# Optimization experiments

Measured on AMD Instinct MI355X. Metric: run time of the kernel, lower is better.

Reference implementation:

```python
import jax, jax.numpy as jnp
import numpy as np

CAPACITY_FACTOR = 1.25


def setup_inputs() -> dict:
    key = jax.random.key(0)
    k1, k2, k3, k4, k5, k6 = jax.random.split(key, 6)
    N, d, E, h = 8192, 1024, 8, 2816
    x = jax.random.normal(k1, (N, d), dtype=jnp.float32)
    topK_indices = jax.random.randint(k2, (N,), 0, E, dtype=jnp.int64)
    topK_scores = jax.random.uniform(k3, (N,), dtype=jnp.float32)
    Wg = jax.random.normal(k4, (E, d, h), dtype=jnp.float32) * 0.02
    Wu = jax.random.normal(k5, (E, d, h), dtype=jnp.float32) * 0.02
    Wd = jax.random.normal(k6, (E, h, d), dtype=jnp.float32) * 0.02
    return {"x": x, "topK_indices": topK_indices, "topK_scores": topK_scores,
            "Wg": Wg, "Wu": Wu, "Wd": Wd}


def reference(x, topK_indices, topK_scores, Wg, Wu, Wd):
    # x: [N, d] tokens; topK_indices: [N] top-1 expert ids; per-expert SwiGLU FFN.
    N, d = x.shape
    E = Wg.shape[0]
    capacity = int(CAPACITY_FACTOR * N / E)  # = 1280

    idx = topK_indices.astype(jnp.int32)
    onehot = jax.nn.one_hot(idx, E, dtype=jnp.int32)            # [N, E]
    # position of each token within its expert's queue (first-come-first-served)
    pos = jnp.sum((jnp.cumsum(onehot, axis=0) - 1) * onehot, axis=1)  # [N]
    kept = pos < capacity                                        # dropped tokens pass through

    # flat dispatch slot: expert*capacity + pos for kept tokens, overflow bucket otherwise
    slots = jnp.where(kept, idx * capacity + pos, E * capacity)  # [N]
    buf = jnp.zeros((E * capacity + 1, d), dtype=x.dtype).at[slots].set(x)
    xe = buf[: E * capacity].reshape(E, capacity, d)             # [E, C, d]

    # per-expert SwiGLU FFN (grouped GEMMs)
    hgate = jnp.einsum('ecd,edh->ech', xe, Wg)
    hup = jnp.einsum('ecd,edh->ech', xe, Wu)
    hact = jax.nn.silu(hgate) * hup
    out = jnp.einsum('ech,ehd->ecd', hact, Wd).reshape(E * capacity, d)
    out = jnp.concatenate([out, jnp.zeros((1, d), out.dtype)], axis=0)

    y_tok = out[slots]                                           # gather back per token
    # multiply_gate_scores=True: scale expert output by routing score; dropped -> identity
    y = jnp.where(kept[:, None], y_tok * topK_scores[:, None], x)
    return y
```

## Files before the change

kernel.cpp:

```cpp
#include <hip/hip_runtime.h>
#include <cstdint>
#include <cstddef>

#define N_TOK 8192
#define DIM   1024
#define NEXP  8
#define HID   2816
#define CAP   1280

typedef __bf16 bf16x8 __attribute__((ext_vector_type(8)));
typedef float  floatx4 __attribute__((ext_vector_type(4)));
typedef unsigned short u16x8 __attribute__((ext_vector_type(8)));

__device__ __forceinline__ unsigned short f2bf(float f) {
  return __builtin_bit_cast(unsigned short, (__bf16)f);
}

__device__ __forceinline__ void async16(void* lds, const void* g) {
  __builtin_amdgcn_global_load_lds(
      (const __attribute__((address_space(1))) void*)g,
      (__attribute__((address_space(3))) void*)lds, 16, 0, 0);
}

__device__ __forceinline__ void fence_barrier() {
  asm volatile("" ::: "memory");
  __builtin_amdgcn_s_barrier();
  asm volatile("" ::: "memory");
}

__device__ __forceinline__ floatx4 mfma16(bf16x8 a, bf16x8 b, floatx4 c) {
  return __builtin_amdgcn_mfma_f32_16x16x32_bf16(a, b, c, 0, 0, 0);
}

__global__ void route_kernel(const int* __restrict__ idx, int idx_stride,
                             int* __restrict__ slot,
                             int* __restrict__ slot_token,
                             int* __restrict__ counts) {
  __shared__ int hist[256][NEXP];
  const int t = threadIdx.x;
  int loc[NEXP];
#pragma unroll
  for (int e = 0; e < NEXP; e++) loc[e] = 0;
  const int base = t * 32;
  for (int i = 0; i < 32; i++) {
    const int e = idx[(base + i) * idx_stride];
#pragma unroll
    for (int k = 0; k < NEXP; k++) loc[k] += (e == k) ? 1 : 0;
  }
  int v[NEXP];
#pragma unroll
  for (int e = 0; e < NEXP; e++) { v[e] = loc[e]; hist[t][e] = loc[e]; }
  __syncthreads();
  for (int d = 1; d < 256; d <<= 1) {
    int nb[NEXP];
    const bool has = (t >= d);
    if (has) {
#pragma unroll
      for (int e = 0; e < NEXP; e++) nb[e] = hist[t - d][e];
    }
    __syncthreads();
    if (has) {
#pragma unroll
      for (int e = 0; e < NEXP; e++) { v[e] += nb[e]; hist[t][e] = v[e]; }
    }
    __syncthreads();
  }
  if (t < NEXP) {
    const int tot = hist[255][t];
    counts[t] = tot < CAP ? tot : CAP;
  }
  int b2[NEXP];
#pragma unroll
  for (int e = 0; e < NEXP; e++) b2[e] = v[e] - loc[e];
  for (int i = 0; i < 32; i++) {
    const int n = base + i;
    const int e = idx[n * idx_stride];
    int p = 0;
#pragma unroll
    for (int k = 0; k < NEXP; k++) {
      if (e == k) { p = b2[k]; b2[k] = p + 1; }
    }
    if (p < CAP) {
      const int s = e * CAP + p;
      slot[n] = s;
      slot_token[s] = n;
    } else {
      slot[n] = -1;
    }
  }
}

__global__ void dispatch_kernel(const float* __restrict__ x,
                                const int* __restrict__ slot,
                                unsigned short* __restrict__ xe,
                                float* __restrict__ y) {
  const int n = blockIdx.x;
  const int t = threadIdx.x;
  const int s = slot[n];
  const float4 v = ((const float4*)(x + (size_t)n * DIM))[t];
  if (s >= 0) {
    ushort4 b;
    b.x = f2bf(v.x); b.y = f2bf(v.y); b.z = f2bf(v.z); b.w = f2bf(v.w);
    ((ushort4*)(xe + (size_t)s * DIM))[t] = b;
  } else {
    ((float4*)(y + (size_t)n * DIM))[t] = v;
  }
}

__global__ __launch_bounds__(256)
void transpose_cvt(const float* __restrict__ in,
                   unsigned short* __restrict__ out,
                   const int R, const int C) {
  __shared__ float tile[64][65];
  const int e = blockIdx.z;
  const float* ib = in + (size_t)e * R * C;
  unsigned short* ob = out + (size_t)e * R * C;
  const int t = threadIdx.x;
  const int c0 = blockIdx.x * 64, r0 = blockIdx.y * 64;
  const int lr = t >> 4;
  const int lc = (t & 15) * 4;
#pragma unroll
  for (int i = 0; i < 4; i++) {
    const float4 v = *(const float4*)(ib + (size_t)(r0 + lr + i * 16) * C + c0 + lc);
    tile[lr + i * 16][lc + 0] = v.x;
    tile[lr + i * 16][lc + 1] = v.y;
    tile[lr + i * 16][lc + 2] = v.z;
    tile[lr + i * 16][lc + 3] = v.w;
  }
  __syncthreads();
  const int oc = t >> 2;
  const int sub = t & 3;
#pragma unroll
  for (int half = 0; half < 2; half++) {
    const int rch = sub + half * 4;
    u16x8 o;
#pragma unroll
    for (int j = 0; j < 8; j++) o[j] = f2bf(tile[rch * 8 + j][oc]);
    *(u16x8*)(ob + (size_t)(c0 + oc) * R + r0 + rch * 8) = o;
  }
}


__global__ __launch_bounds__(512, 2)
void gateup_gemm4(const unsigned short* __restrict__ A,
                  const unsigned short* __restrict__ Bg,
                  const unsigned short* __restrict__ Bu,
                  const int* __restrict__ counts,
                  unsigned short* __restrict__ hact) {
  extern __shared__ __align__(16) char smem[];
  const int bid = blockIdx.x;
  const int xcd = bid & 7;
  const int slotb = bid >> 3;
  const int m = slotb % 5;
  const int cgl = slotb / 5;
  const int cg = xcd + 8 * cgl;
  const int n = cg % 44;
  const int e = cg / 44;

  const int cnt = counts[e];
  const int m0 = m * 256;
  if (m0 >= cnt) return;
  const int n0 = n * 64;

  const int t = threadIdx.x;
  const int lane = t & 63;
  const int w = t >> 6;
  const int wr = w >> 1;
  const int wc = w & 1;
  const int li = lane & 15;
  const int q = lane >> 4;

  const int cphys = (((li & 1) * 4 + q) ^ (li >> 1)) * 16;
  const int aoff0 = (wr * 32 + (li >> 1)) * 128 + cphys;
  const int boff0 = 16384 + (wc * 16 + (li >> 1)) * 128 + cphys;

  const int clog = (t & 7) ^ ((t >> 3) & 7);
  const int kc = (clog & 3) * 8;
  const int rloc = 2 * (t >> 3) + (clog >> 2);
  const unsigned short* aSrc  = A + ((size_t)e * CAP + m0 + rloc) * DIM + kc;
  const unsigned short* aSrc2 = aSrc + (size_t)128 * DIM;
  const int rB = n0 + 2 * ((t >> 3) & 31) + (clog >> 2);
  const unsigned short* bSrc =
      ((t < 256) ? Bg : Bu) + ((size_t)e * HID + rB) * DIM + kc;

  floatx4 accg[4][2] = {};
  floatx4 accu[4][2] = {};
  bf16x8 fA[8], fB[8];

  constexpr int NTK = DIM / 32;

#define GU_STAGE(TN)                                                        \
  {                                                                         \
    char* bb_ = smem + ((TN) & 3) * 24576;                                  \
    const int ko_ = (TN) * 32;                                              \
    async16(bb_ + t * 16, aSrc + ko_);                                      \
    async16(bb_ + 8192 + t * 16, aSrc2 + ko_);                              \
    async16(bb_ + 16384 + t * 16, bSrc + ko_);                              \
  }

#define GU_READF(DST, TN)                                                   \
  {                                                                         \
    const char* sb_ = smem + ((TN) & 3) * 24576;                            \
    DST[0] = *(const bf16x8*)(sb_ + aoff0);                                 \
    DST[1] = *(const bf16x8*)(sb_ + aoff0 + 1024);                          \
    DST[2] = *(const bf16x8*)(sb_ + aoff0 + 2048);                          \
    DST[3] = *(const bf16x8*)(sb_ + aoff0 + 3072);                          \
    DST[4] = *(const bf16x8*)(sb_ + boff0);                                 \
    DST[5] = *(const bf16x8*)(sb_ + boff0 + 1024);                          \
    DST[6] = *(const bf16x8*)(sb_ + boff0 + 4096);                          \
    DST[7] = *(const bf16x8*)(sb_ + boff0 + 5120);                          \
  }

#define GU_MFMA(CUR)                                                        \
  {                                                                         \
    __builtin_amdgcn_s_setprio(1);                                          \
    _Pragma("unroll")                                                       \
    for (int mi = 0; mi < 4; mi++) {                                        \
      accg[mi][0] = mfma16(CUR[mi], CUR[4], accg[mi][0]);                   \
      accg[mi][1] = mfma16(CUR[mi], CUR[5], accg[mi][1]);                   \
      accu[mi][0] = mfma16(CUR[mi], CUR[6], accu[mi][0]);                   \
      accu[mi][1] = mfma16(CUR[mi], CUR[7], accu[mi][1]);                   \
    }                                                                       \
    __builtin_amdgcn_s_setprio(0);                                          \
  }

#define GU_BODY(TN, CUR, NXT)                                               \
  {                                                                         \
    if ((TN) + 3 < NTK) GU_STAGE((TN) + 3);                                 \
    if ((TN) + 1 < NTK) {                                                   \
      if ((TN) + 3 < NTK)      asm volatile("s_waitcnt vmcnt(6)" ::: "memory"); \
      else if ((TN) + 2 < NTK) asm volatile("s_waitcnt vmcnt(3)" ::: "memory"); \
      else                     asm volatile("s_waitcnt vmcnt(0)" ::: "memory"); \
      fence_barrier();                                                      \
      GU_READF(NXT, (TN) + 1);                                              \
      __builtin_amdgcn_sched_barrier(0);                                    \
    }                                                                       \
    GU_MFMA(CUR);                                                           \
    asm volatile("s_waitcnt lgkmcnt(0)" ::: "memory");                      \
    __builtin_amdgcn_sched_barrier(0);                                      \
  }

  GU_STAGE(0); GU_STAGE(1); GU_STAGE(2);
  asm volatile("s_waitcnt vmcnt(6)" ::: "memory");
  fence_barrier();
  GU_READF(fA, 0);
  asm volatile("s_waitcnt lgkmcnt(0)" ::: "memory");
  __builtin_amdgcn_sched_barrier(0);

  for (int T = 0; T < NTK; T += 2) {
    GU_BODY(T, fA, fB);
    GU_BODY(T + 1, fB, fA);
  }
#undef GU_BODY
#undef GU_MFMA
#undef GU_READF
#undef GU_STAGE

  unsigned short* ob = hact + (size_t)e * CAP * HID;
#pragma unroll
  for (int mi = 0; mi < 4; mi++)
#pragma unroll
    for (int r = 0; r < 4; r++) {
      const int row = m0 + wr * 64 + mi * 16 + q * 4 + r;
      const size_t rb = (size_t)row * HID;
#pragma unroll
      for (int ni = 0; ni < 2; ni++) {
        const int col = n0 + wc * 32 + ni * 16 + li;
        const float g = accg[mi][ni][r];
        const float u = accu[mi][ni][r];
        ob[rb + col] = f2bf(g / (1.0f + __expf(-g)) * u);
      }
    }
}

__global__ __launch_bounds__(256, 2)
void down_gemm4(const unsigned short* __restrict__ Ah,
                const unsigned short* __restrict__ Bt,
                const int* __restrict__ counts,
                const int* __restrict__ slot_token,
                const float* __restrict__ scores,
                float* __restrict__ y) {
  extern __shared__ __align__(16) char smem[];
  const int bid = blockIdx.x;
  const int xcd = bid & 7;
  const int slotb = bid >> 3;
  const int m = slotb % 10;
  const int cgl = slotb / 10;
  const int cg = xcd + 8 * cgl;
  const int n = cg % 8;
  const int e = cg / 8;

  const int cnt = counts[e];
  const int m0 = m * 128;
  if (m0 >= cnt) return;
  const int n0 = n * 128;

  const int t = threadIdx.x;
  const int lane = t & 63;
  const int w = t >> 6;
  const int wr = w >> 1;
  const int wc = w & 1;
  const int li = lane & 15;
  const int q = lane >> 4;

  const int cphys = (((li & 1) * 4 + q) ^ (li >> 1)) * 16;
  const int aoff0 = (wr * 32 + (li >> 1)) * 128 + cphys;
  const int boff0 = 8192 + (wc * 32 + (li >> 1)) * 128 + cphys;

  const int clog = (t & 7) ^ ((t >> 3) & 7);
  const int kc = (clog & 3) * 8;
  const int rloc = 2 * (t >> 3) + (clog >> 2);
  const unsigned short* aSrc  = Ah + ((size_t)e * CAP + m0 + rloc) * HID + kc;
  const unsigned short* aSrc2 = aSrc + (size_t)64 * HID;
  const unsigned short* bSrc  = Bt + ((size_t)e * DIM + n0 + rloc) * HID + kc;
  const unsigned short* bSrc2 = bSrc + (size_t)64 * HID;

  floatx4 acc[4][4] = {};
  bf16x8 fA[8], fB[8];

  constexpr int NTK = HID / 32;

#define DN_STAGE(TN)                                                        \
  {                                                                         \
    char* bb_ = smem + ((TN) & 3) * 16384;                                  \
    const int ko_ = (TN) * 32;                                              \
    async16(bb_ + t * 16, aSrc + ko_);                                      \
    async16(bb_ + 4096 + t * 16, aSrc2 + ko_);                              \
    async16(bb_ + 8192 + t * 16, bSrc + ko_);                               \
    async16(bb_ + 12288 + t * 16, bSrc2 + ko_);                             \
  }

#define DN_READF(DST, TN)                                                   \
  {                                                                         \
    const char* sb_ = smem + ((TN) & 3) * 16384;                            \
    DST[0] = *(const bf16x8*)(sb_ + aoff0);                                 \
    DST[1] = *(const bf16x8*)(sb_ + aoff0 + 1024);                          \
    DST[2] = *(const bf16x8*)(sb_ + aoff0 + 2048);                          \
    DST[3] = *(const bf16x8*)(sb_ + aoff0 + 3072);                          \
    DST[4] = *(const bf16x8*)(sb_ + boff0);                                 \
    DST[5] = *(const bf16x8*)(sb_ + boff0 + 1024);                          \
    DST[6] = *(const bf16x8*)(sb_ + boff0 + 2048);                          \
    DST[7] = *(const bf16x8*)(sb_ + boff0 + 3072);                          \
  }

#define DN_MFMA(CUR)                                                        \
  {                                                                         \
    __builtin_amdgcn_s_setprio(1);                                          \
    _Pragma("unroll")                                                       \
    for (int mi = 0; mi < 4; mi++) {                                        \
      _Pragma("unroll")                                                     \
      for (int ni = 0; ni < 4; ni++)                                        \
        acc[mi][ni] = mfma16(CUR[mi], CUR[4 + ni], acc[mi][ni]);            \
    }                                                                       \
    __builtin_amdgcn_s_setprio(0);                                          \
  }

#define DN_BODY(TN, CUR, NXT)                                               \
  {                                                                         \
    if ((TN) + 3 < NTK) DN_STAGE((TN) + 3);                                 \
    if ((TN) + 1 < NTK) {                                                   \
      if ((TN) + 3 < NTK)      asm volatile("s_waitcnt vmcnt(8)" ::: "memory"); \
      else if ((TN) + 2 < NTK) asm volatile("s_waitcnt vmcnt(4)" ::: "memory"); \
      else                     asm volatile("s_waitcnt vmcnt(0)" ::: "memory"); \
      fence_barrier();                                                      \
      DN_READF(NXT, (TN) + 1);                                              \
      __builtin_amdgcn_sched_barrier(0);                                    \
    }                                                                       \
    DN_MFMA(CUR);                                                           \
    asm volatile("s_waitcnt lgkmcnt(0)" ::: "memory");                      \
    __builtin_amdgcn_sched_barrier(0);                                      \
  }

  DN_STAGE(0); DN_STAGE(1); DN_STAGE(2);
  asm volatile("s_waitcnt vmcnt(8)" ::: "memory");
  fence_barrier();
  DN_READF(fA, 0);
  asm volatile("s_waitcnt lgkmcnt(0)" ::: "memory");
  __builtin_amdgcn_sched_barrier(0);

  for (int T = 0; T < NTK; T += 2) {
    DN_BODY(T, fA, fB);
    DN_BODY(T + 1, fB, fA);
  }
#undef DN_BODY
#undef DN_MFMA
#undef DN_READF
#undef DN_STAGE

#pragma unroll
  for (int mi = 0; mi < 4; mi++)
#pragma unroll
    for (int r = 0; r < 4; r++) {
      const int row = m0 + wr * 64 + mi * 16 + q * 4 + r;
      if (row < cnt) {
        const int tok = slot_token[e * CAP + row];
        const float s = scores[tok];
        float* yr = y + (size_t)tok * DIM;
#pragma unroll
        for (int ni = 0; ni < 4; ni++) {
          const int col = n0 + wc * 64 + ni * 16 + li;
          yr[col] = acc[mi][ni][r] * s;
        }
      }
    }
}

extern "C" void kernel_launch(void* const* d_in, const int* in_sizes, int n_in,
                              void* d_out, int out_size, void* d_ws, size_t ws_size,
                              hipStream_t stream) {
  const float* x      = (const float*)d_in[0];
  const int*   idx    = (const int*)d_in[1];
  const float* scores = (const float*)d_in[2];
  const float* Wg     = (const float*)d_in[3];
  const float* Wu     = (const float*)d_in[4];
  const float* Wd     = (const float*)d_in[5];
  float* y = (float*)d_out;

  const int idx_stride = (in_sizes[1] == 2 * N_TOK) ? 2 : 1;

  char* ws = (char*)d_ws;
  size_t off = 0;
  auto alloc = [&](size_t b) -> char* {
    char* p = ws + off;
    off += (b + 255) & ~(size_t)255;
    return p;
  };
  int* counts            = (int*)alloc(NEXP * 4);
  int* slot              = (int*)alloc((size_t)N_TOK * 4);
  int* slot_token        = (int*)alloc((size_t)NEXP * CAP * 4);
  unsigned short* xe     = (unsigned short*)alloc((size_t)NEXP * CAP * DIM * 2);
  unsigned short* hact   = (unsigned short*)alloc((size_t)NEXP * CAP * HID * 2);
  unsigned short* wg_t   = (unsigned short*)alloc((size_t)NEXP * DIM * HID * 2);
  unsigned short* wu_t   = (unsigned short*)alloc((size_t)NEXP * DIM * HID * 2);
  unsigned short* wd_t   = (unsigned short*)alloc((size_t)NEXP * DIM * HID * 2);
  (void)ws_size; (void)n_in; (void)out_size;

  static bool s_attr_done = false;
  if (!s_attr_done) {
    hipFuncSetAttribute((const void*)gateup_gemm4,
                        hipFuncAttributeMaxDynamicSharedMemorySize, 98304);
    hipFuncSetAttribute((const void*)down_gemm4,
                        hipFuncAttributeMaxDynamicSharedMemorySize, 65536);
    s_attr_done = true;
  }

  route_kernel<<<1, 256, 0, stream>>>(idx, idx_stride, slot, slot_token, counts);
  dispatch_kernel<<<N_TOK, 256, 0, stream>>>(x, slot, xe, y);

  transpose_cvt<<<dim3(HID / 64, DIM / 64, NEXP), 256, 0, stream>>>(Wg, wg_t, DIM, HID);
  transpose_cvt<<<dim3(HID / 64, DIM / 64, NEXP), 256, 0, stream>>>(Wu, wu_t, DIM, HID);
  transpose_cvt<<<dim3(DIM / 64, HID / 64, NEXP), 256, 0, stream>>>(Wd, wd_t, HID, DIM);

  gateup_gemm4<<<8 * 44 * 5, 512, 98304, stream>>>(xe, wg_t, wu_t, counts, hact);
  down_gemm4<<<8 * 8 * 10, 256, 65536, stream>>>(hact, wd_t, counts, slot_token, scores, y);
}
```

Before: 561.7 us.

## Widen gate/up tile to 128 cols, triple-buffer both GEMMs, expert-per-XCD mapping

The gate/up GEMM tile grows from 64 to 128 hidden columns with a 2x4 warp layout, so each A tile is reused across twice as many columns and the grid is halved. Both GEMMs move from a 4-stage, double-register-fragment pipeline to a 3-stage LDS ring that loads fragments and issues MFMAs in the same iteration. The down GEMM drops to 48KB of LDS so three blocks can fit per CU. Blocks are remapped so each XCD handles a single expert, which is meant to improve L2 reuse of that expert's weights. In exchange, the gate/up kernel needs more accumulator registers and loses the overlap between fragment reads and MFMAs that the old prefetch scheme gave.

```diff
diff --git a/kernel.cpp b/kernel.cpp
--- a/kernel.cpp
+++ b/kernel.cpp
@@ -142,126 +142,97 @@
 
 
 __global__ __launch_bounds__(512, 2)
-void gateup_gemm4(const unsigned short* __restrict__ A,
+void gateup_gemm5(const unsigned short* __restrict__ A,
                   const unsigned short* __restrict__ Bg,
                   const unsigned short* __restrict__ Bu,
                   const int* __restrict__ counts,
                   unsigned short* __restrict__ hact) {
   extern __shared__ __align__(16) char smem[];
   const int bid = blockIdx.x;
-  const int xcd = bid & 7;
-  const int slotb = bid >> 3;
-  const int m = slotb % 5;
-  const int cgl = slotb / 5;
-  const int cg = xcd + 8 * cgl;
-  const int n = cg % 44;
-  const int e = cg / 44;
+  const int e = bid & 7;
+  const int local = bid >> 3;
+  const int n = local / 5;
+  const int m = local % 5;
 
   const int cnt = counts[e];
   const int m0 = m * 256;
   if (m0 >= cnt) return;
-  const int n0 = n * 64;
+  const int n0 = n * 128;
 
   const int t = threadIdx.x;
   const int lane = t & 63;
   const int w = t >> 6;
-  const int wr = w >> 1;
-  const int wc = w & 1;
+  const int wr = w >> 2;
+  const int wc = w & 3;
   const int li = lane & 15;
   const int q = lane >> 4;
 
   const int cphys = (((li & 1) * 4 + q) ^ (li >> 1)) * 16;
-  const int aoff0 = (wr * 32 + (li >> 1)) * 128 + cphys;
-  const int boff0 = 16384 + (wc * 16 + (li >> 1)) * 128 + cphys;
+  const int aoff0 = wr * 8192 + (li >> 1) * 128 + cphys;
+  const int bgoff = 16384 + wc * 2048 + (li >> 1) * 128 + cphys;
+  const int buoff = bgoff + 8192;
 
   const int clog = (t & 7) ^ ((t >> 3) & 7);
   const int kc = (clog & 3) * 8;
   const int rloc = 2 * (t >> 3) + (clog >> 2);
-  const unsigned short* aSrc  = A + ((size_t)e * CAP + m0 + rloc) * DIM + kc;
-  const unsigned short* aSrc2 = aSrc + (size_t)128 * DIM;
-  const int rB = n0 + 2 * ((t >> 3) & 31) + (clog >> 2);
-  const unsigned short* bSrc =
-      ((t < 256) ? Bg : Bu) + ((size_t)e * HID + rB) * DIM + kc;
-
-  floatx4 accg[4][2] = {};
-  floatx4 accu[4][2] = {};
-  bf16x8 fA[8], fB[8];
+  const unsigned short* aS0 = A  + ((size_t)e * CAP + m0 + rloc) * DIM + kc;
+  const unsigned short* aS1 = aS0 + (size_t)128 * DIM;
+  const unsigned short* bgS = Bg + ((size_t)e * HID + n0 + rloc) * DIM + kc;
+  const unsigned short* buS = Bu + ((size_t)e * HID + n0 + rloc) * DIM + kc;
+
+  floatx4 accg[8][2] = {};
+  floatx4 accu[8][2] = {};
 
   constexpr int NTK = DIM / 32;
 
 #define GU_STAGE(TN)                                                        \
   {                                                                         \
-    char* bb_ = smem + ((TN) & 3) * 24576;                                  \
+    char* bb_ = smem + ((TN) % 3) * 32768;                                  \
     const int ko_ = (TN) * 32;                                              \
-    async16(bb_ + t * 16, aSrc + ko_);                                      \
-    async16(bb_ + 8192 + t * 16, aSrc2 + ko_);                              \
-    async16(bb_ + 16384 + t * 16, bSrc + ko_);                              \
-  }
-
-#define GU_READF(DST, TN)                                                   \
-  {                                                                         \
-    const char* sb_ = smem + ((TN) & 3) * 24576;                            \
-    DST[0] = *(const bf16x8*)(sb_ + aoff0);                                 \
-    DST[1] = *(const bf16x8*)(sb_ + aoff0 + 1024);                          \
-    DST[2] = *(const bf16x8*)(sb_ + aoff0 + 2048);                          \
-    DST[3] = *(const bf16x8*)(sb_ + aoff0 + 3072);                          \
-    DST[4] = *(const bf16x8*)(sb_ + boff0);                                 \
-    DST[5] = *(const bf16x8*)(sb_ + boff0 + 1024);                          \
-    DST[6] = *(const bf16x8*)(sb_ + boff0 + 4096);                          \
-    DST[7] = *(const bf16x8*)(sb_ + boff0 + 5120);                          \
-  }
-
-#define GU_MFMA(CUR)                                                        \
-  {                                                                         \
-    __builtin_amdgcn_s_setprio(1);                                          \
-    _Pragma("unroll")                                                       \
-    for (int mi = 0; mi < 4; mi++) {                                        \
-      accg[mi][0] = mfma16(CUR[mi], CUR[4], accg[mi][0]);                   \
-      accg[mi][1] = mfma16(CUR[mi], CUR[5], accg[mi][1]);                   \
-      accu[mi][0] = mfma16(CUR[mi], CUR[6], accu[mi][0]);                   \
-      accu[mi][1] = mfma16(CUR[mi], CUR[7], accu[mi][1]);                   \
-    }                                                                       \
-    __builtin_amdgcn_s_setprio(0);                                          \
-  }
-
-#define GU_BODY(TN, CUR, NXT)                                               \
-  {                                                                         \
-    if ((TN) + 3 < NTK) GU_STAGE((TN) + 3);                                 \
-    if ((TN) + 1 < NTK) {                                                   \
-      if ((TN) + 3 < NTK)      asm volatile("s_waitcnt vmcnt(6)" ::: "memory"); \
-      else if ((TN) + 2 < NTK) asm volatile("s_waitcnt vmcnt(3)" ::: "memory"); \
-      else                     asm volatile("s_waitcnt vmcnt(0)" ::: "memory"); \
-      fence_barrier();                                                      \
-      GU_READF(NXT, (TN) + 1);                                              \
-      __builtin_amdgcn_sched_barrier(0);                                    \
-    }                                                                       \
-    GU_MFMA(CUR);                                                           \
-    asm volatile("s_waitcnt lgkmcnt(0)" ::: "memory");                      \
-    __builtin_amdgcn_sched_barrier(0);                                      \
-  }
-
-  GU_STAGE(0); GU_STAGE(1); GU_STAGE(2);
-  asm volatile("s_waitcnt vmcnt(6)" ::: "memory");
-  fence_barrier();
-  GU_READF(fA, 0);
-  asm volatile("s_waitcnt lgkmcnt(0)" ::: "memory");
-  __builtin_amdgcn_sched_barrier(0);
-
-  for (int T = 0; T < NTK; T += 2) {
-    GU_BODY(T, fA, fB);
-    GU_BODY(T + 1, fB, fA);
-  }
-#undef GU_BODY
-#undef GU_MFMA
-#undef GU_READF
+    async16(bb_ + t * 16, aS0 + ko_);                                       \
+    async16(bb_ + 8192 + t * 16, aS1 + ko_);                                \
+    async16(bb_ + 16384 + t * 16, bgS + ko_);                               \
+    async16(bb_ + 24576 + t * 16, buS + ko_);                               \
+  }
+
+  GU_STAGE(0);
+  GU_STAGE(1);
+
+  for (int T = 0; T < NTK; T++) {
+    if (T + 1 < NTK) asm volatile("s_waitcnt vmcnt(4)" ::: "memory");
+    else             asm volatile("s_waitcnt vmcnt(0)" ::: "memory");
+    fence_barrier();
+    const char* sb = smem + (T % 3) * 32768;
+    bf16x8 fa[8], fg[2], fu[2];
+#pragma unroll
+    for (int mi = 0; mi < 8; mi++)
+      fa[mi] = *(const bf16x8*)(sb + aoff0 + mi * 1024);
+#pragma unroll
+    for (int ni = 0; ni < 2; ni++) {
+      fg[ni] = *(const bf16x8*)(sb + bgoff + ni * 1024);
+      fu[ni] = *(const bf16x8*)(sb + buoff + ni * 1024);
+    }
+    if (T + 2 < NTK) GU_STAGE(T + 2);
+    asm volatile("s_waitcnt lgkmcnt(0)" ::: "memory");
+    __builtin_amdgcn_sched_barrier(0);
+    __builtin_amdgcn_s_setprio(1);
+#pragma unroll
+    for (int mi = 0; mi < 8; mi++) {
+      accg[mi][0] = mfma16(fa[mi], fg[0], accg[mi][0]);
+      accg[mi][1] = mfma16(fa[mi], fg[1], accg[mi][1]);
+      accu[mi][0] = mfma16(fa[mi], fu[0], accu[mi][0]);
+      accu[mi][1] = mfma16(fa[mi], fu[1], accu[mi][1]);
+    }
+    __builtin_amdgcn_s_setprio(0);
+  }
 #undef GU_STAGE
 
   unsigned short* ob = hact + (size_t)e * CAP * HID;
 #pragma unroll
-  for (int mi = 0; mi < 4; mi++)
+  for (int mi = 0; mi < 8; mi++)
 #pragma unroll
     for (int r = 0; r < 4; r++) {
-      const int row = m0 + wr * 64 + mi * 16 + q * 4 + r;
+      const int row = m0 + wr * 128 + mi * 16 + q * 4 + r;
       const size_t rb = (size_t)row * HID;
 #pragma unroll
       for (int ni = 0; ni < 2; ni++) {
@@ -273,8 +244,8 @@
     }
 }
 
-__global__ __launch_bounds__(256, 2)
-void down_gemm4(const unsigned short* __restrict__ Ah,
+__global__ __launch_bounds__(256, 3)
+void down_gemm5(const unsigned short* __restrict__ Ah,
                 const unsigned short* __restrict__ Bt,
                 const int* __restrict__ counts,
                 const int* __restrict__ slot_token,
@@ -282,13 +253,10 @@
                 float* __restrict__ y) {
   extern __shared__ __align__(16) char smem[];
   const int bid = blockIdx.x;
-  const int xcd = bid & 7;
-  const int slotb = bid >> 3;
-  const int m = slotb % 10;
-  const int cgl = slotb / 10;
-  const int cg = xcd + 8 * cgl;
-  const int n = cg % 8;
-  const int e = cg / 8;
+  const int e = bid & 7;
+  const int local = bid >> 3;
+  const int n = local / 10;
+  const int m = local % 10;
 
   const int cnt = counts[e];
   const int m0 = m * 128;
@@ -304,87 +272,57 @@
   const int q = lane >> 4;
 
   const int cphys = (((li & 1) * 4 + q) ^ (li >> 1)) * 16;
-  const int aoff0 = (wr * 32 + (li >> 1)) * 128 + cphys;
-  const int boff0 = 8192 + (wc * 32 + (li >> 1)) * 128 + cphys;
+  const int aoff0 = wr * 4096 + (li >> 1) * 128 + cphys;
+  const int boff0 = 8192 + wc * 4096 + (li >> 1) * 128 + cphys;
 
   const int clog = (t & 7) ^ ((t >> 3) & 7);
   const int kc = (clog & 3) * 8;
   const int rloc = 2 * (t >> 3) + (clog >> 2);
-  const unsigned short* aSrc  = Ah + ((size_t)e * CAP + m0 + rloc) * HID + kc;
-  const unsigned short* aSrc2 = aSrc + (size_t)64 * HID;
-  const unsigned short* bSrc  = Bt + ((size_t)e * DIM + n0 + rloc) * HID + kc;
-  const unsigned short* bSrc2 = bSrc + (size_t)64 * HID;
+  const unsigned short* aS0 = Ah + ((size_t)e * CAP + m0 + rloc) * HID + kc;
+  const unsigned short* aS1 = aS0 + (size_t)64 * HID;
+  const unsigned short* bS0 = Bt + ((size_t)e * DIM + n0 + rloc) * HID + kc;
+  const unsigned short* bS1 = bS0 + (size_t)64 * HID;
 
   floatx4 acc[4][4] = {};
-  bf16x8 fA[8], fB[8];
 
   constexpr int NTK = HID / 32;
 
 #define DN_STAGE(TN)                                                        \
   {                                                                         \
-    char* bb_ = smem + ((TN) & 3) * 16384;                                  \
+    char* bb_ = smem + ((TN) % 3) * 16384;                                  \
     const int ko_ = (TN) * 32;                                              \
-    async16(bb_ + t * 16, aSrc + ko_);                                      \
-    async16(bb_ + 4096 + t * 16, aSrc2 + ko_);                              \
-    async16(bb_ + 8192 + t * 16, bSrc + ko_);                               \
-    async16(bb_ + 12288 + t * 16, bSrc2 + ko_);                             \
-  }
-
-#define DN_READF(DST, TN)                                                   \
-  {                                                                         \
-    const char* sb_ = smem + ((TN) & 3) * 16384;                            \
-    DST[0] = *(const bf16x8*)(sb_ + aoff0);                                 \
-    DST[1] = *(const bf16x8*)(sb_ + aoff0 + 1024);                          \
-    DST[2] = *(const bf16x8*)(sb_ + aoff0 + 2048);                          \
-    DST[3] = *(const bf16x8*)(sb_ + aoff0 + 3072);                          \
-    DST[4] = *(const bf16x8*)(sb_ + boff0);                                 \
-    DST[5] = *(const bf16x8*)(sb_ + boff0 + 1024);                          \
-    DST[6] = *(const bf16x8*)(sb_ + boff0 + 2048);                          \
-    DST[7] = *(const bf16x8*)(sb_ + boff0 + 3072);                          \
-  }
-
-#define DN_MFMA(CUR)                                                        \
-  {                                                                         \
-    __builtin_amdgcn_s_setprio(1);                                          \
-    _Pragma("unroll")                                                       \
-    for (int mi = 0; mi < 4; mi++) {                                        \
-      _Pragma("unroll")                                                     \
-      for (int ni = 0; ni < 4; ni++)                                        \
-        acc[mi][ni] = mfma16(CUR[mi], CUR[4 + ni], acc[mi][ni]);            \
-    }                                                                       \
-    __builtin_amdgcn_s_setprio(0);                                          \
-  }
-
-#define DN_BODY(TN, CUR, NXT)                                               \
-  {                                                                         \
-    if ((TN) + 3 < NTK) DN_STAGE((TN) + 3);                                 \
-    if ((TN) + 1 < NTK) {                                                   \
-      if ((TN) + 3 < NTK)      asm volatile("s_waitcnt vmcnt(8)" ::: "memory"); \
-      else if ((TN) + 2 < NTK) asm volatile("s_waitcnt vmcnt(4)" ::: "memory"); \
-      else                     asm volatile("s_waitcnt vmcnt(0)" ::: "memory"); \
-      fence_barrier();                                                      \
-      DN_READF(NXT, (TN) + 1);                                              \
-      __builtin_amdgcn_sched_barrier(0);                                    \
-    }                                                                       \
-    DN_MFMA(CUR);                                                           \
-    asm volatile("s_waitcnt lgkmcnt(0)" ::: "memory");                      \
-    __builtin_amdgcn_sched_barrier(0);                                      \
-  }
-
-  DN_STAGE(0); DN_STAGE(1); DN_STAGE(2);
-  asm volatile("s_waitcnt vmcnt(8)" ::: "memory");
-  fence_barrier();
-  DN_READF(fA, 0);
-  asm volatile("s_waitcnt lgkmcnt(0)" ::: "memory");
-  __builtin_amdgcn_sched_barrier(0);
-
-  for (int T = 0; T < NTK; T += 2) {
-    DN_BODY(T, fA, fB);
-    DN_BODY(T + 1, fB, fA);
-  }
-#undef DN_BODY
-#undef DN_MFMA
-#undef DN_READF
+    async16(bb_ + t * 16, aS0 + ko_);                                       \
+    async16(bb_ + 4096 + t * 16, aS1 + ko_);                                \
+    async16(bb_ + 8192 + t * 16, bS0 + ko_);                                \
+    async16(bb_ + 12288 + t * 16, bS1 + ko_);                               \
+  }
+
+  DN_STAGE(0);
+  DN_STAGE(1);
+
+  for (int T = 0; T < NTK; T++) {
+    if (T + 1 < NTK) asm volatile("s_waitcnt vmcnt(4)" ::: "memory");
+    else             asm volatile("s_waitcnt vmcnt(0)" ::: "memory");
+    fence_barrier();
+    const char* sb = smem + (T % 3) * 16384;
+    bf16x8 fa[4], fb[4];
+#pragma unroll
+    for (int mi = 0; mi < 4; mi++)
+      fa[mi] = *(const bf16x8*)(sb + aoff0 + mi * 1024);
+#pragma unroll
+    for (int ni = 0; ni < 4; ni++)
+      fb[ni] = *(const bf16x8*)(sb + boff0 + ni * 1024);
+    if (T + 2 < NTK) DN_STAGE(T + 2);
+    asm volatile("s_waitcnt lgkmcnt(0)" ::: "memory");
+    __builtin_amdgcn_sched_barrier(0);
+    __builtin_amdgcn_s_setprio(1);
+#pragma unroll
+    for (int mi = 0; mi < 4; mi++)
+#pragma unroll
+      for (int ni = 0; ni < 4; ni++)
+        acc[mi][ni] = mfma16(fa[mi], fb[ni], acc[mi][ni]);
+    __builtin_amdgcn_s_setprio(0);
+  }
 #undef DN_STAGE
 
 #pragma unroll
@@ -437,10 +375,10 @@
 
   static bool s_attr_done = false;
   if (!s_attr_done) {
-    hipFuncSetAttribute((const void*)gateup_gemm4,
+    hipFuncSetAttribute((const void*)gateup_gemm5,
                         hipFuncAttributeMaxDynamicSharedMemorySize, 98304);
-    hipFuncSetAttribute((const void*)down_gemm4,
-                        hipFuncAttributeMaxDynamicSharedMemorySize, 65536);
+    hipFuncSetAttribute((const void*)down_gemm5,
+                        hipFuncAttributeMaxDynamicSharedMemorySize, 49152);
     s_attr_done = true;
   }
 
@@ -451,6 +389,6 @@
   transpose_cvt<<<dim3(HID / 64, DIM / 64, NEXP), 256, 0, stream>>>(Wu, wu_t, DIM, HID);
   transpose_cvt<<<dim3(DIM / 64, HID / 64, NEXP), 256, 0, stream>>>(Wd, wd_t, HID, DIM);
 
-  gateup_gemm4<<<8 * 44 * 5, 512, 98304, stream>>>(xe, wg_t, wu_t, counts, hact);
-  down_gemm4<<<8 * 8 * 10, 256, 65536, stream>>>(hact, wd_t, counts, slot_token, scores, y);
-}
+  gateup_gemm5<<<8 * 22 * 5, 512, 98304, stream>>>(xe, wg_t, wu_t, counts, hact);
+  down_gemm5<<<8 * 8 * 10, 256, 49152, stream>>>(hact, wd_t, counts, slot_token, scores, y);
+}
```

Result: faster. 541.1 us (-3.7%).
